# Optimization experiments

Hardware: AMD Instinct MI355X
Metric: run time of the kernel (lower is better)

## Reference

```python
import jax, jax.numpy as jnp
import numpy as np

BETA = 0.9       # neuron_args['beta']
THRESH = 0.5     # neuron_args['threshold'] (mem_thresh)
ALPHA = 2.0      # surrogate.atan(alpha=2)
BIN = 50         # int(0.2 / 0.004)
NSTEPS = 7       # num_steps
STEP = BIN // NSTEPS  # 7 -> only buffer[:49] is used


@jax.custom_vjp
def atan_spike(x):
    return (x > 0).astype(x.dtype)

def _asp_fwd(x):
    return (x > 0).astype(x.dtype), x

def _asp_bwd(x, g):
    return (g * (ALPHA / 2.0) / (1.0 + (jnp.pi / 2.0 * ALPHA * x) ** 2),)

atan_spike.defvjp(_asp_fwd, _asp_bwd)


def _heaviside_detached(x):
    # snntorch mem_reset: reset = spike_grad(mem - thresh).detach()
    return jax.lax.stop_gradient((x > 0).astype(x.dtype))


def _forward(x, W_in, W_h0, W_out, v_x, v_y):
    T, B, D = x.shape
    H = W_in.shape[0]
    O = W_out.shape[0]
    vxy = jnp.concatenate([v_x, v_y])  # (2,)

    def single_forward(acc):  # acc: (NSTEPS, B, D)
        mem1 = jnp.zeros((B, H), x.dtype)
        mem2 = jnp.zeros((B, H), x.dtype)
        mem_out = jnp.zeros((B, O), x.dtype)
        for s in range(NSTEPS):
            cur = acc[s] @ W_in.T                      # (B, H); dropout in eval mode = identity
            reset = _heaviside_detached(mem1 - THRESH)
            mem1 = (BETA * mem1 + cur) * (1.0 - reset)  # reset_mechanism='zero'
            spk = atan_spike(mem1 - THRESH)
            cur = spk @ W_h0.T
            reset = _heaviside_detached(mem2 - THRESH)
            mem2 = (BETA * mem2 + cur) * (1.0 - reset)
            spk = atan_spike(mem2 - THRESH)
            cur = spk @ W_out.T                        # (B, O)
            mem_out = BETA * mem_out + cur             # reset_mechanism='none'
        return mem_out

    def step(carry, x_t):
        buf, L = carry  # buf: (BIN, B, D) zero-padded past L valid frames
        # torch: append then trim front when >BIN. While growing, frames keep
        # fixed positions with zeros at the end (NOT a sliding window yet).
        grow = jax.lax.dynamic_update_slice_in_dim(buf, x_t[None], L, 0)
        slide = jnp.concatenate([buf[1:], x_t[None]], axis=0)
        buf = jnp.where(L < BIN, grow, slide)
        L = jnp.minimum(L + 1, BIN)
        # acc_spikes[i] = sum(buf[7i : 7i+7]); frame 49 unused (49 = 7*7)
        acc = buf[: NSTEPS * STEP].reshape(NSTEPS, STEP, B, D).sum(axis=1)
        pred = single_forward(acc)                     # (B, 2)
        return (buf, L), pred * vxy

    init = (jnp.zeros((BIN, B, D), x.dtype), jnp.int32(1))  # one initial zero frame
    _, preds = jax.lax.scan(step, init, x)             # (T, B, 2)
    return preds


def setup_inputs() -> dict:
    key = jax.random.key(0)
    ks = jax.random.split(key, 6)
    T, B, D, H, O = 128, 1024, 96, 128, 2
    x = jax.random.uniform(ks[0], (T, B, D), dtype=jnp.float32)
    W_in = jax.random.normal(ks[1], (H, D), dtype=jnp.float32) / np.sqrt(D)
    W_h0 = jax.random.normal(ks[2], (H, H), dtype=jnp.float32) / np.sqrt(H)
    W_out = jax.random.normal(ks[3], (O, H), dtype=jnp.float32) / np.sqrt(H)
    v_x = jax.random.normal(ks[4], (1,), dtype=jnp.float32)
    v_y = jax.random.normal(ks[5], (1,), dtype=jnp.float32)
    return {"x": x, "W_in": W_in, "W_h0": W_h0, "W_out": W_out, "v_x": v_x, "v_y": v_y}


def reference(x, W_in, W_h0, W_out, v_x, v_y):
    return _forward(x, W_in, W_h0, W_out, v_x, v_y)
```

## Files before the change

### kernel.cpp

```cpp
#include <hip/hip_runtime.h>
#include <cstdint>

#define T_STEPS 128
#define BATCH   1024
#define D_INPUT 96
#define H_DIM   128
#define NWIN    163
#define BD      (BATCH * D_INPUT)

__device__ __forceinline__ int widx_for(int t, int s) {
    if (t >= 49) return t - 49 + 7 * s;
    if (s == 0)  return 121 + min(5, t);
    const int st = 7 * s - 1;
    if (t < st) return -1;
    const int len = min(7, t - st + 1);
    return (len == 7) ? st : (127 + (s - 1) * 6 + (len - 1));
}

__device__ __forceinline__ int swz_idx(int row, int col) {
    return (row << 7) | (col ^ ((row & 63) << 1));
}

__global__ __launch_bounds__(256) void kT_wint(const float* __restrict__ Win,
                                               const float* __restrict__ Wh0,
                                               float* __restrict__ WinT,
                                               float* __restrict__ Wh0Q) {
    const int tid = threadIdx.x;
    if (blockIdx.x < 48) {
        const int e = blockIdx.x * 256 + tid;
        const int h = e / D_INPUT, d = e % D_INPUT;
        WinT[d * H_DIM + h] = Win[e];
    } else {
        const int e = (blockIdx.x - 48) * 256 + tid;
        const int r = e & 3, p = (e >> 2) & 1, q = (e >> 3) & 31, j = e >> 8;
        Wh0Q[e] = Wh0[(4 * q + r) * H_DIM + (2 * j + p)];
    }
}

__global__ __launch_bounds__(256) void kA0_winsum(const float* __restrict__ x,
                                                  float* __restrict__ WS) {
    const int flat = blockIdx.x * 256 + threadIdx.x;
    float* wsp = WS + flat;
    float r[7];
#pragma unroll
    for (int t = 0; t < T_STEPS; ++t) {
        r[t % 7] = x[(size_t)t * BD + flat];
        if (t <= 5) {
            float s = r[0];
#pragma unroll
            for (int k = 1; k <= t; ++k) s = __fadd_rn(s, r[k % 7]);
            wsp[(size_t)(121 + t) * BD] = s;
        }
        if (t >= 6 && t <= 126) {
            const int w = t - 6;
            float s = r[w % 7];
#pragma unroll
            for (int k = 1; k < 7; ++k) s = __fadd_rn(s, r[(w + k) % 7]);
            wsp[(size_t)w * BD] = s;
        }
        if (t >= 6 && t <= 46) {
            const int sv = (t + 1) / 7;
            if (sv >= 1 && 7 * sv >= t - 4 && 7 * sv <= t + 1) {
                const int start = 7 * sv - 1;
                const int len = t - start + 1;
                float s = r[start % 7];
#pragma unroll
                for (int k = 1; k < len; ++k) s = __fadd_rn(s, r[(start + k) % 7]);
                wsp[(size_t)(127 + (sv - 1) * 6 + (len - 1)) * BD] = s;
            }
        }
    }
}

__global__ __launch_bounds__(256) void kA_wincur(const float* __restrict__ WS,
                                                 const float* __restrict__ WinT,
                                                 float* __restrict__ CUR1) {
    __shared__ float xs[D_INPUT * 32];
    __shared__ float wT[D_INPUT * H_DIM];
    const int widx = blockIdx.x;
    const int b0   = blockIdx.y * 32;
    const int tid  = threadIdx.x;

    {
        const float2* WinT2 = (const float2*)WinT;
        for (int e2 = tid; e2 < D_INPUT * (H_DIM / 2); e2 += 256) {
            const int d = e2 >> 6, h2 = e2 & 63;
            *(float2*)&wT[swz_idx(d, h2 << 1)] = WinT2[e2];
        }
    }
    for (int e = tid; e < D_INPUT * 32; e += 256) {
        const int d = e % D_INPUT, bq = e / D_INPUT;
        xs[d * 32 + bq] = WS[(size_t)widx * BD + (size_t)(b0 + bq) * D_INPUT + d];
    }
    __syncthreads();

    const int hp = tid & 63, g = tid >> 6;
    const int h0 = hp << 1;
    float acc[8][2];
#pragma unroll
    for (int r = 0; r < 8; ++r) { acc[r][0] = 0.f; acc[r][1] = 0.f; }

#pragma unroll 6
    for (int d = 0; d < D_INPUT; ++d) {
        const float2 wp  = *(const float2*)&wT[swz_idx(d, h0)];
        const float4 xv0 = *(const float4*)&xs[d * 32 + g * 8];
        const float4 xv1 = *(const float4*)&xs[d * 32 + g * 8 + 4];
        const float xv[8] = {xv0.x,xv0.y,xv0.z,xv0.w, xv1.x,xv1.y,xv1.z,xv1.w};
#pragma unroll
        for (int r = 0; r < 8; ++r) {
            acc[r][0] = __fmaf_rn(xv[r], wp.x, acc[r][0]);
            acc[r][1] = __fmaf_rn(xv[r], wp.y, acc[r][1]);
        }
    }
    float* op = CUR1 + ((size_t)widx * BATCH + b0 + g * 8) * H_DIM + h0;
#pragma unroll
    for (int r = 0; r < 8; ++r) {
        float2 o; o.x = acc[r][0]; o.y = acc[r][1];
        *(float2*)(op + (size_t)r * H_DIM) = o;
    }
}

__global__ __launch_bounds__(512, 2) void kB_snn(const float* __restrict__ CUR1,
                                                 const float* __restrict__ Wh0Q,
                                                 const float* __restrict__ Wout,
                                                 const float* __restrict__ vxp,
                                                 const float* __restrict__ vyp,
                                                 float* __restrict__ out) {
    __shared__ float sf[8][64 * 32];
    const int tid = threadIdx.x;

    const int w = tid >> 6, lane = tid & 63;
    const int t  = blockIdx.y;
    const int i0 = lane << 1;
    const int g  = lane >> 5;
    const int q  = lane & 31;
    const int iq = q << 2;
    float* sfw = sf[w];
    const int lbase = lane * 32;
    const float4 wex4 = *(const float4*)&Wout[iq];
    const float4 wey4 = *(const float4*)&Wout[H_DIM + iq];
    const float vx = vxp[0], vy = vyp[0];
    const int b0 = (blockIdx.x << 7) + (w << 4);

    float m1a[16], m1b[16], c1a[16], c1b[16];
    bool  s1a[16], s1b[16];
    float m2[8][4], po0[8], po1[8];
    bool  s2[8][4];
#pragma unroll
    for (int k = 0; k < 16; ++k) {
        m1a[k]=0.f; m1b[k]=0.f; s1a[k]=false; s1b[k]=false;
    }
#pragma unroll
    for (int b = 0; b < 8; ++b) {
        po0[b]=0.f; po1[b]=0.f;
#pragma unroll
        for (int r = 0; r < 4; ++r) { m2[b][r]=0.f; s2[b][r]=false; }
    }

    {
        const int wi = widx_for(t, 0);
#pragma unroll
        for (int k = 0; k < 16; ++k) {
            c1a[k] = 0.f; c1b[k] = 0.f;
            if (wi >= 0) {
                const float2 v = *(const float2*)
                    &CUR1[((size_t)wi * BATCH + b0 + k) * H_DIM + i0];
                c1a[k] = v.x; c1b[k] = v.y;
            }
        }
    }

#pragma unroll 1
    for (int s = 0; s < 7; ++s) {
        float sev[16], sov[16];
#pragma unroll
        for (int k = 0; k < 16; ++k) {
            m1a[k] = s1a[k] ? 0.f : __fadd_rn(__fmul_rn(0.9f, m1a[k]), c1a[k]);
            m1b[k] = s1b[k] ? 0.f : __fadd_rn(__fmul_rn(0.9f, m1b[k]), c1b[k]);
            s1a[k] = m1a[k] > 0.5f; s1b[k] = m1b[k] > 0.5f;
            sev[k] = s1a[k] ? 1.0f : 0.0f;
            sov[k] = s1b[k] ? 1.0f : 0.0f;
        }
#pragma unroll
        for (int c = 0; c < 4; ++c) {
            float4 v;
            v.x = sev[c*4]; v.y = sev[c*4+1]; v.z = sev[c*4+2]; v.w = sev[c*4+3];
            *(float4*)&sfw[lbase + ((c     ^ (lane & 7)) << 2)] = v;
            v.x = sov[c*4]; v.y = sov[c*4+1]; v.z = sov[c*4+2]; v.w = sov[c*4+3];
            *(float4*)&sfw[lbase + (((c+4) ^ (lane & 7)) << 2)] = v;
        }

        const int win = (s < 6) ? widx_for(t, s + 1) : -1;
#pragma unroll
        for (int k = 0; k < 16; ++k) {
            c1a[k] = 0.f; c1b[k] = 0.f;
            if (win >= 0) {
                const float2 v = *(const float2*)
                    &CUR1[((size_t)win * BATCH + b0 + k) * H_DIM + i0];
                c1a[k] = v.x; c1b[k] = v.y;
            }
        }

        float c2[8][4];
#pragma unroll
        for (int b = 0; b < 8; ++b)
#pragma unroll
            for (int r = 0; r < 4; ++r) c2[b][r] = 0.f;

#pragma unroll 8
        for (int j = 0; j < 64; ++j) {
            const float4 we4 = *(const float4*)&Wh0Q[((size_t)(j * 32 + q)) * 8];
            const float4 wo4 = *(const float4*)&Wh0Q[((size_t)(j * 32 + q)) * 8 + 4];
            const int jb = j * 32, jx = (j & 7) << 2;
            const float4 E0 = *(const float4*)&sfw[jb + (((2*g    ) << 2) ^ jx)];
            const float4 E1 = *(const float4*)&sfw[jb + (((2*g + 1) << 2) ^ jx)];
            const float4 O0 = *(const float4*)&sfw[jb + (((2*g + 4) << 2) ^ jx)];
            const float4 O1 = *(const float4*)&sfw[jb + (((2*g + 5) << 2) ^ jx)];
            const float sevj[8] = {E0.x,E0.y,E0.z,E0.w, E1.x,E1.y,E1.z,E1.w};
            const float sovj[8] = {O0.x,O0.y,O0.z,O0.w, O1.x,O1.y,O1.z,O1.w};
            const float wev[4] = {we4.x, we4.y, we4.z, we4.w};
            const float wov[4] = {wo4.x, wo4.y, wo4.z, wo4.w};
#pragma unroll
            for (int b = 0; b < 8; ++b) {
#pragma unroll
                for (int r = 0; r < 4; ++r) {
                    c2[b][r] = __fmaf_rn(sevj[b], wev[r], c2[b][r]);
                    c2[b][r] = __fmaf_rn(sovj[b], wov[r], c2[b][r]);
                }
            }
        }

#pragma unroll
        for (int b = 0; b < 8; ++b) {
            float p0 = 0.f, p1 = 0.f;
#pragma unroll
            for (int r = 0; r < 4; ++r) {
                m2[b][r] = s2[b][r] ? 0.f
                         : __fadd_rn(__fmul_rn(0.9f, m2[b][r]), c2[b][r]);
                s2[b][r] = m2[b][r] > 0.5f;
                p0 += s2[b][r] ? ((const float*)&wex4)[r] : 0.f;
                p1 += s2[b][r] ? ((const float*)&wey4)[r] : 0.f;
            }
            po0[b] = __fmaf_rn(0.9f, po0[b], p0);
            po1[b] = __fmaf_rn(0.9f, po1[b], p1);
        }
    }

#pragma unroll
    for (int b = 0; b < 8; ++b) {
        float r0 = po0[b], r1 = po1[b];
#pragma unroll
        for (int off = 16; off > 0; off >>= 1) {
            r0 += __shfl_xor(r0, off);
            r1 += __shfl_xor(r1, off);
        }
        if (q == 0) {
            float2 o;
            o.x = __fmul_rn(r0, vx);
            o.y = __fmul_rn(r1, vy);
            *(float2*)(out + ((size_t)t * BATCH + b0 + g * 8 + b) * 2) = o;
        }
    }
}

extern "C" void kernel_launch(void* const* d_in, const int* in_sizes, int n_in,
                              void* d_out, int out_size, void* d_ws, size_t ws_size,
                              hipStream_t stream) {
    const float* x    = (const float*)d_in[0];
    const float* Win  = (const float*)d_in[1];
    const float* Wh0  = (const float*)d_in[2];
    const float* Wout = (const float*)d_in[3];
    const float* vx   = (const float*)d_in[4];
    const float* vy   = (const float*)d_in[5];
    float* out  = (float*)d_out;

    float* CUR1 = (float*)d_ws;
    float* WS   = CUR1 + (size_t)NWIN * BATCH * H_DIM;
    float* WinT = WS   + (size_t)NWIN * BATCH * D_INPUT;
    float* Wh0Q = WinT + (size_t)D_INPUT * H_DIM;

    kT_wint   <<<dim3(112),                 dim3(256), 0, stream>>>(Win, Wh0, WinT, Wh0Q);
    kA0_winsum<<<dim3(BD / 256),            dim3(256), 0, stream>>>(x, WS);
    kA_wincur <<<dim3(NWIN, BATCH / 32),    dim3(256), 0, stream>>>(WS, WinT, CUR1);
    kB_snn    <<<dim3(BATCH / 128, T_STEPS), dim3(512), 0, stream>>>(CUR1, Wh0Q, Wout, vx, vy, out);
}
```

Before: 828.9 us.

## Retile input projection and hidden GEMM for wider per-thread register blocking

The input-projection kernel now handles 64 batch rows per block, with each thread producing an 8x4 output block. The Win tile in shared memory is permuted so threads can read weight pairs and write float4 results, and the x tile uses an XOR swizzle. In the SNN kernel, each thread now computes 4 batch rows by 8 hidden units instead of 8 by 4. Wh0 is re-laid out so each thread reads 16 contiguous weights per j, halving shared spike loads per FMA and shortening the reduction shuffle. The trade-offs are more weight traffic per thread and different register pressure and occupancy.

```diff
diff --git a/kernel.cpp b/kernel.cpp
--- a/kernel.cpp
+++ b/kernel.cpp
@@ -17,14 +17,10 @@
     return (len == 7) ? st : (127 + (s - 1) * 6 + (len - 1));
 }
 
-__device__ __forceinline__ int swz_idx(int row, int col) {
-    return (row << 7) | (col ^ ((row & 63) << 1));
-}
-
 __global__ __launch_bounds__(256) void kT_wint(const float* __restrict__ Win,
                                                const float* __restrict__ Wh0,
                                                float* __restrict__ WinT,
-                                               float* __restrict__ Wh0Q) {
+                                               float* __restrict__ Wh0O) {
     const int tid = threadIdx.x;
     if (blockIdx.x < 48) {
         const int e = blockIdx.x * 256 + tid;
@@ -32,8 +28,8 @@
         WinT[d * H_DIM + h] = Win[e];
     } else {
         const int e = (blockIdx.x - 48) * 256 + tid;
-        const int r = e & 3, p = (e >> 2) & 1, q = (e >> 3) & 31, j = e >> 8;
-        Wh0Q[e] = Wh0[(4 * q + r) * H_DIM + (2 * j + p)];
+        const int r = e & 7, p = (e >> 3) & 1, q = (e >> 4) & 15, j = e >> 8;
+        Wh0O[e] = Wh0[(8 * q + r) * H_DIM + (2 * j + p)];
     }
 }
 
@@ -75,53 +71,63 @@
 __global__ __launch_bounds__(256) void kA_wincur(const float* __restrict__ WS,
                                                  const float* __restrict__ WinT,
                                                  float* __restrict__ CUR1) {
-    __shared__ float xs[D_INPUT * 32];
-    __shared__ float wT[D_INPUT * H_DIM];
+    __shared__ float xs[D_INPUT * 64];
+    __shared__ float wq[D_INPUT * H_DIM];
     const int widx = blockIdx.x;
-    const int b0   = blockIdx.y * 32;
+    const int b0   = blockIdx.y * 64;
     const int tid  = threadIdx.x;
 
     {
         const float2* WinT2 = (const float2*)WinT;
-        for (int e2 = tid; e2 < D_INPUT * (H_DIM / 2); e2 += 256) {
-            const int d = e2 >> 6, h2 = e2 & 63;
-            *(float2*)&wT[swz_idx(d, h2 << 1)] = WinT2[e2];
-        }
-    }
-    for (int e = tid; e < D_INPUT * 32; e += 256) {
-        const int d = e % D_INPUT, bq = e / D_INPUT;
-        xs[d * 32 + bq] = WS[(size_t)widx * BD + (size_t)(b0 + bq) * D_INPUT + d];
+        for (int e2 = tid; e2 < D_INPUT * 64; e2 += 256) {
+            const int p = e2 & 63, d = e2 >> 6;
+            *(float2*)&wq[d * 128 + ((p & 1) << 6) + ((p >> 1) << 1)] = WinT2[e2];
+        }
+    }
+    for (int e = tid; e < D_INPUT * 64; e += 256) {
+        const int d = e % 96, bq = e / 96;
+        xs[d * 64 + (bq ^ (d & 24))] =
+            WS[(size_t)widx * BD + (size_t)(b0 + bq) * 96 + d];
     }
     __syncthreads();
 
-    const int hp = tid & 63, g = tid >> 6;
-    const int h0 = hp << 1;
-    float acc[8][2];
-#pragma unroll
-    for (int r = 0; r < 8; ++r) { acc[r][0] = 0.f; acc[r][1] = 0.f; }
-
-#pragma unroll 6
+    const int q  = tid & 31;
+    const int g  = (tid >> 5) & 1;
+    const int w  = tid >> 6;
+    const int ob = (w << 1) | g;
+
+    float acc[8][4];
+#pragma unroll
+    for (int r = 0; r < 8; ++r)
+#pragma unroll
+        for (int hh = 0; hh < 4; ++hh) acc[r][hh] = 0.f;
+
+#pragma unroll 4
     for (int d = 0; d < D_INPUT; ++d) {
-        const float2 wp  = *(const float2*)&wT[swz_idx(d, h0)];
-        const float4 xv0 = *(const float4*)&xs[d * 32 + g * 8];
-        const float4 xv1 = *(const float4*)&xs[d * 32 + g * 8 + 4];
+        const float2 wp0 = *(const float2*)&wq[d * 128 + 2 * q];
+        const float2 wp1 = *(const float2*)&wq[d * 128 + 64 + 2 * q];
+        const int xb = d * 64 + ((ob * 8) ^ (d & 24));
+        const float4 xv0 = *(const float4*)&xs[xb];
+        const float4 xv1 = *(const float4*)&xs[xb + 4];
         const float xv[8] = {xv0.x,xv0.y,xv0.z,xv0.w, xv1.x,xv1.y,xv1.z,xv1.w};
 #pragma unroll
         for (int r = 0; r < 8; ++r) {
-            acc[r][0] = __fmaf_rn(xv[r], wp.x, acc[r][0]);
-            acc[r][1] = __fmaf_rn(xv[r], wp.y, acc[r][1]);
-        }
-    }
-    float* op = CUR1 + ((size_t)widx * BATCH + b0 + g * 8) * H_DIM + h0;
+            acc[r][0] = __fmaf_rn(xv[r], wp0.x, acc[r][0]);
+            acc[r][1] = __fmaf_rn(xv[r], wp0.y, acc[r][1]);
+            acc[r][2] = __fmaf_rn(xv[r], wp1.x, acc[r][2]);
+            acc[r][3] = __fmaf_rn(xv[r], wp1.y, acc[r][3]);
+        }
+    }
+    float* op = CUR1 + ((size_t)widx * BATCH + b0 + ob * 8) * H_DIM + 4 * q;
 #pragma unroll
     for (int r = 0; r < 8; ++r) {
-        float2 o; o.x = acc[r][0]; o.y = acc[r][1];
-        *(float2*)(op + (size_t)r * H_DIM) = o;
+        float4 o; o.x = acc[r][0]; o.y = acc[r][1]; o.z = acc[r][2]; o.w = acc[r][3];
+        *(float4*)(op + (size_t)r * H_DIM) = o;
     }
 }
 
 __global__ __launch_bounds__(512, 2) void kB_snn(const float* __restrict__ CUR1,
-                                                 const float* __restrict__ Wh0Q,
+                                                 const float* __restrict__ Wh0O,
                                                  const float* __restrict__ Wout,
                                                  const float* __restrict__ vxp,
                                                  const float* __restrict__ vyp,
@@ -132,29 +138,33 @@
     const int w = tid >> 6, lane = tid & 63;
     const int t  = blockIdx.y;
     const int i0 = lane << 1;
-    const int g  = lane >> 5;
-    const int q  = lane & 31;
-    const int iq = q << 2;
+    const int g2 = lane >> 4;
+    const int q  = lane & 15;
     float* sfw = sf[w];
     const int lbase = lane * 32;
-    const float4 wex4 = *(const float4*)&Wout[iq];
-    const float4 wey4 = *(const float4*)&Wout[H_DIM + iq];
+    const float4 wea = *(const float4*)&Wout[q * 8];
+    const float4 web = *(const float4*)&Wout[q * 8 + 4];
+    const float4 woa = *(const float4*)&Wout[H_DIM + q * 8];
+    const float4 wob = *(const float4*)&Wout[H_DIM + q * 8 + 4];
+    const float wex[8] = {wea.x,wea.y,wea.z,wea.w, web.x,web.y,web.z,web.w};
+    const float wey[8] = {woa.x,woa.y,woa.z,woa.w, wob.x,wob.y,wob.z,wob.w};
     const float vx = vxp[0], vy = vyp[0];
     const int b0 = (blockIdx.x << 7) + (w << 4);
+    const float* wbase = Wh0O + q * 16;
 
     float m1a[16], m1b[16], c1a[16], c1b[16];
     bool  s1a[16], s1b[16];
-    float m2[8][4], po0[8], po1[8];
-    bool  s2[8][4];
+    float m2[4][8], po0[4], po1[4];
+    bool  s2[4][8];
 #pragma unroll
     for (int k = 0; k < 16; ++k) {
         m1a[k]=0.f; m1b[k]=0.f; s1a[k]=false; s1b[k]=false;
     }
 #pragma unroll
-    for (int b = 0; b < 8; ++b) {
+    for (int b = 0; b < 4; ++b) {
         po0[b]=0.f; po1[b]=0.f;
 #pragma unroll
-        for (int r = 0; r < 4; ++r) { m2[b][r]=0.f; s2[b][r]=false; }
+        for (int r = 0; r < 8; ++r) { m2[b][r]=0.f; s2[b][r]=false; }
     }
 
     {
@@ -201,45 +211,46 @@
             }
         }
 
-        float c2[8][4];
-#pragma unroll
-        for (int b = 0; b < 8; ++b)
-#pragma unroll
-            for (int r = 0; r < 4; ++r) c2[b][r] = 0.f;
+        float c2[4][8];
+#pragma unroll
+        for (int b = 0; b < 4; ++b)
+#pragma unroll
+            for (int r = 0; r < 8; ++r) c2[b][r] = 0.f;
 
 #pragma unroll 8
         for (int j = 0; j < 64; ++j) {
-            const float4 we4 = *(const float4*)&Wh0Q[((size_t)(j * 32 + q)) * 8];
-            const float4 wo4 = *(const float4*)&Wh0Q[((size_t)(j * 32 + q)) * 8 + 4];
-            const int jb = j * 32, jx = (j & 7) << 2;
-            const float4 E0 = *(const float4*)&sfw[jb + (((2*g    ) << 2) ^ jx)];
-            const float4 E1 = *(const float4*)&sfw[jb + (((2*g + 1) << 2) ^ jx)];
-            const float4 O0 = *(const float4*)&sfw[jb + (((2*g + 4) << 2) ^ jx)];
-            const float4 O1 = *(const float4*)&sfw[jb + (((2*g + 5) << 2) ^ jx)];
-            const float sevj[8] = {E0.x,E0.y,E0.z,E0.w, E1.x,E1.y,E1.z,E1.w};
-            const float sovj[8] = {O0.x,O0.y,O0.z,O0.w, O1.x,O1.y,O1.z,O1.w};
-            const float wev[4] = {we4.x, we4.y, we4.z, we4.w};
-            const float wov[4] = {wo4.x, wo4.y, wo4.z, wo4.w};
-#pragma unroll
-            for (int b = 0; b < 8; ++b) {
-#pragma unroll
-                for (int r = 0; r < 4; ++r) {
-                    c2[b][r] = __fmaf_rn(sevj[b], wev[r], c2[b][r]);
-                    c2[b][r] = __fmaf_rn(sovj[b], wov[r], c2[b][r]);
+            const float* wj = wbase + (size_t)j * 256;
+            const float4 wa = *(const float4*)&wj[0];
+            const float4 wb = *(const float4*)&wj[4];
+            const float4 wc = *(const float4*)&wj[8];
+            const float4 wd = *(const float4*)&wj[12];
+            const int jb = j * 32, js = j & 7;
+            const float4 E = *(const float4*)&sfw[jb + (((g2    ) ^ js) << 2)];
+            const float4 O = *(const float4*)&sfw[jb + (((g2 + 4) ^ js) << 2)];
+            const float seb[4] = {E.x, E.y, E.z, E.w};
+            const float sob[4] = {O.x, O.y, O.z, O.w};
+            const float wev[8] = {wa.x,wa.y,wa.z,wa.w, wb.x,wb.y,wb.z,wb.w};
+            const float wov[8] = {wc.x,wc.y,wc.z,wc.w, wd.x,wd.y,wd.z,wd.w};
+#pragma unroll
+            for (int b = 0; b < 4; ++b) {
+#pragma unroll
+                for (int r = 0; r < 8; ++r) {
+                    c2[b][r] = __fmaf_rn(seb[b], wev[r], c2[b][r]);
+                    c2[b][r] = __fmaf_rn(sob[b], wov[r], c2[b][r]);
                 }
             }
         }
 
 #pragma unroll
-        for (int b = 0; b < 8; ++b) {
+        for (int b = 0; b < 4; ++b) {
             float p0 = 0.f, p1 = 0.f;
 #pragma unroll
-            for (int r = 0; r < 4; ++r) {
+            for (int r = 0; r < 8; ++r) {
                 m2[b][r] = s2[b][r] ? 0.f
                          : __fadd_rn(__fmul_rn(0.9f, m2[b][r]), c2[b][r]);
                 s2[b][r] = m2[b][r] > 0.5f;
-                p0 += s2[b][r] ? ((const float*)&wex4)[r] : 0.f;
-                p1 += s2[b][r] ? ((const float*)&wey4)[r] : 0.f;
+                p0 += s2[b][r] ? wex[r] : 0.f;
+                p1 += s2[b][r] ? wey[r] : 0.f;
             }
             po0[b] = __fmaf_rn(0.9f, po0[b], p0);
             po1[b] = __fmaf_rn(0.9f, po1[b], p1);
@@ -247,10 +258,10 @@
     }
 
 #pragma unroll
-    for (int b = 0; b < 8; ++b) {
+    for (int b = 0; b < 4; ++b) {
         float r0 = po0[b], r1 = po1[b];
 #pragma unroll
-        for (int off = 16; off > 0; off >>= 1) {
+        for (int off = 8; off > 0; off >>= 1) {
             r0 += __shfl_xor(r0, off);
             r1 += __shfl_xor(r1, off);
         }
@@ -258,7 +269,7 @@
             float2 o;
             o.x = __fmul_rn(r0, vx);
             o.y = __fmul_rn(r1, vy);
-            *(float2*)(out + ((size_t)t * BATCH + b0 + g * 8 + b) * 2) = o;
+            *(float2*)(out + ((size_t)t * BATCH + b0 + g2 * 4 + b) * 2) = o;
         }
     }
 }
@@ -277,10 +288,10 @@
     float* CUR1 = (float*)d_ws;
     float* WS   = CUR1 + (size_t)NWIN * BATCH * H_DIM;
     float* WinT = WS   + (size_t)NWIN * BATCH * D_INPUT;
-    float* Wh0Q = WinT + (size_t)D_INPUT * H_DIM;
-
-    kT_wint   <<<dim3(112),                 dim3(256), 0, stream>>>(Win, Wh0, WinT, Wh0Q);
-    kA0_winsum<<<dim3(BD / 256),            dim3(256), 0, stream>>>(x, WS);
-    kA_wincur <<<dim3(NWIN, BATCH / 32),    dim3(256), 0, stream>>>(WS, WinT, CUR1);
-    kB_snn    <<<dim3(BATCH / 128, T_STEPS), dim3(512), 0, stream>>>(CUR1, Wh0Q, Wout, vx, vy, out);
-}
+    float* Wh0O = WinT + (size_t)D_INPUT * H_DIM;
+
+    kT_wint   <<<dim3(112),                  dim3(256), 0, stream>>>(Win, Wh0, WinT, Wh0O);
+    kA0_winsum<<<dim3(BD / 256),             dim3(256), 0, stream>>>(x, WS);
+    kA_wincur <<<dim3(NWIN, BATCH / 64),     dim3(256), 0, stream>>>(WS, WinT, CUR1);
+    kB_snn    <<<dim3(BATCH / 128, T_STEPS), dim3(512), 0, stream>>>(CUR1, Wh0O, Wout, vx, vy, out);
+}
```

Result: slower. 1.204 ms (+45.2%).
